# Optimization experiments

Measured on AMD Instinct MI355X. Metric: run time of the kernel, lower is better.

The kernel has to match this reference:

```python
import jax, jax.numpy as jnp
import numpy as np

WIN_H = WIN_W = 7
NUM_HEADS = 6
DIM = 192
HEAD_DIM = DIM // NUM_HEADS
NUM_WIN = 1024
B_ = 8192
N = WIN_H * WIN_W


def _relative_position_index(win_h, win_w):
    coords = np.stack(np.meshgrid(np.arange(win_h), np.arange(win_w), indexing='ij'))  # (2,h,w)
    flat = coords.reshape(2, -1)
    rel = flat[:, :, None] - flat[:, None, :]          # (2, N, N)
    rel = rel.transpose(1, 2, 0).astype(np.int32)      # (N, N, 2)
    rel[:, :, 0] += win_h - 1
    rel[:, :, 1] += win_w - 1
    rel[:, :, 0] *= 2 * win_w - 1
    return rel.sum(-1)                                 # (N, N) in [0, (2h-1)(2w-1))


def setup_inputs() -> dict:
    key = jax.random.key(0)
    ks = jax.random.split(key, 7)
    return {
        'x': jax.random.normal(ks[0], (B_, N, DIM), jnp.float32),
        'mask': jax.random.normal(ks[1], (NUM_WIN, N, N), jnp.float32),
        'qkv_w': jax.random.normal(ks[2], (3 * DIM, DIM), jnp.float32) * 0.02,
        'qkv_b': jax.random.normal(ks[3], (3 * DIM,), jnp.float32) * 0.02,
        'proj_w': jax.random.normal(ks[4], (DIM, DIM), jnp.float32) * 0.02,
        'proj_b': jax.random.normal(ks[5], (DIM,), jnp.float32) * 0.02,
        'rpb_table': jax.random.normal(ks[6], ((2 * WIN_H - 1) * (2 * WIN_W - 1), NUM_HEADS), jnp.float32) * 0.02,
        'rel_index': jnp.asarray(_relative_position_index(WIN_H, WIN_W)),
    }


def reference(x, mask, qkv_w, qkv_b, proj_w, proj_b, rpb_table, rel_index):
    B, n, C = x.shape
    H, hd = NUM_HEADS, HEAD_DIM
    scale = hd ** (-0.5)

    qkv = (x @ qkv_w.T + qkv_b).reshape(B, n, 3, H, hd)
    qkv = jnp.transpose(qkv, (2, 0, 3, 1, 4))          # (3, B, H, N, hd)
    q, k, v = qkv[0], qkv[1], qkv[2]

    attn = jnp.einsum('bhnd,bhmd->bhnm', q * scale, k)  # (B, H, N, N)

    # gathered relative position bias: (N*N,) -> (N, N, H) -> (H, N, N)
    bias = rpb_table[rel_index.reshape(-1)].reshape(n, n, H)
    attn = attn + jnp.transpose(bias, (2, 0, 1))[None]

    num_win = mask.shape[0]
    attn = attn.reshape(B // num_win, num_win, H, n, n) + mask[None, :, None]
    attn = jax.nn.softmax(attn, axis=-1).reshape(B, H, n, n)

    out = jnp.einsum('bhnm,bhmd->bhnd', attn, v)         # (B, H, N, hd)
    out = jnp.transpose(out, (0, 2, 1, 3)).reshape(B, n, H * hd)
    return out @ proj_w.T + proj_b
```

## Files before the change

kernel.cpp:

```cpp
#include <hip/hip_runtime.h>

#define NTOK  49
#define NWIN  1024
#define SCALE 0.17677669529663687f

#define SMEM_BYTES 102400

typedef __bf16 bfx8 __attribute__((ext_vector_type(8)));
typedef float  f32x4 __attribute__((ext_vector_type(4)));
typedef unsigned long long ull;
typedef unsigned int uint;

union BF8 { bfx8 v; ull q[2]; };
union BFU { __bf16 h[4]; ull q; };

__device__ __forceinline__ ull pack4(f32x4 a) {
    BFU u;
    u.h[0] = (__bf16)a[0]; u.h[1] = (__bf16)a[1];
    u.h[2] = (__bf16)a[2]; u.h[3] = (__bf16)a[3];
    return u.q;
}
__device__ __forceinline__ unsigned short f2bf(float f) {
    uint u = __builtin_bit_cast(uint, f);
    u += 0x7fffu + ((u >> 16) & 1u);
    return (unsigned short)(u >> 16);
}
__device__ __forceinline__ f32x4 mfma16(bfx8 a, bfx8 b, f32x4 c) {
    return __builtin_amdgcn_mfma_f32_16x16x32_bf16(a, b, c, 0, 0, 0);
}

extern "C" __global__ void wattn_prep(const float* __restrict__ qkv_w,
                                      const float* __restrict__ proj_w,
                                      const float* __restrict__ rpb,
                                      const int*   __restrict__ rel,
                                      const float* __restrict__ qkv_b,
                                      unsigned short* __restrict__ W1f,
                                      unsigned short* __restrict__ W2p,
                                      float* __restrict__ qkvbs,
                                      float* __restrict__ biasN)
{
    const int i = blockIdx.x * 256 + threadIdx.x;
    if (i < 110592) {
        const int e = i & 7, l = (i >> 3) & 63, f = i >> 9;
        const int kk = f % 6, oct = f / 6;
        const int R = oct * 16 + (l & 15), C = kk * 32 + (l >> 4) * 8 + e;
        float v = qkv_w[R * 192 + C];
        if (oct < 12) v *= SCALE;
        W1f[i] = f2bf(v);
    }
    if (i < 36864) {
        const int e = i & 7, l = (i >> 3) & 63, f = i >> 9;
        const int c2t = f / 6, H = f % 6;
        const int R = c2t * 16 + (l & 15);
        const int C = H * 32 + (e >> 2) * 16 + (l >> 4) * 4 + (e & 3);
        W2p[i] = f2bf(proj_w[R * 192 + C]);
    }
    if (i < 576) qkvbs[i] = (i < 192) ? qkv_b[i] * SCALE : qkv_b[i];
    if (i < 6 * NTOK * 64) {
        const int h = i / (NTOK * 64), ii = (i / 64) % NTOK, j = i % 64;
        biasN[i] = (j < NTOK) ? rpb[rel[ii * NTOK + j] * 6 + h] : -1e30f;
    }
}

extern "C" __global__ void __launch_bounds__(512, 2)
wattn_fused(const float* __restrict__ x,
            const float* __restrict__ mask,
            const float* __restrict__ proj_b,
            const unsigned short* __restrict__ W1f,
            const unsigned short* __restrict__ W2p,
            const float* __restrict__ qkvbs,
            const float* __restrict__ biasN,
            float* __restrict__ out)
{
    __shared__ char smem[SMEM_BYTES];
    char* const XB  = smem;
    char* const OBX = smem;
    char* const QBp = smem + 25600;
    char* const KBp = smem + 50176;
    char* const VTp = smem + 74752;

    const int tid  = threadIdx.x;
    const int wave = tid >> 6;
    const int lane = tid & 63;
    const int g    = lane >> 4;
    const int jn   = lane & 15;
    const int qt   = wave & 3;
    const int hh   = wave >> 2;
    const size_t b = blockIdx.x;

#pragma unroll
    for (int u = 0; u < 3; ++u) {
        const int i = tid + u * 512;
        if (i < 1500)
            *(uint*)(XB + (49 + i / 100) * 400 + (i % 100) * 4) = 0u;
    }
    {
        const float4* xw = (const float4*)(x + b * 9408);
#pragma unroll
        for (int u = 0; u < 5; ++u) {
            const int i = tid + u * 512;
            if (i < 2352) {
                float4 v = xw[i];
                f32x4 vv = {v.x, v.y, v.z, v.w};
                *(ull*)(XB + (i / 48) * 400 + (i % 48) * 8) = pack4(vv);
            }
        }
    }
    __syncthreads();

#pragma unroll
    for (int jj = 0; jj < 2; ++jj) {
        const int pr = wave + 8 * jj;
        const int octA = pr * 2;
        bfx8 wfA[6], wfB[6];
#pragma unroll
        for (int kk = 0; kk < 6; ++kk) {
            wfA[kk] = *(const bfx8*)(W1f + ((size_t)(octA * 6 + kk) * 64 + lane) * 8);
            wfB[kk] = *(const bfx8*)(W1f + ((size_t)((octA + 1) * 6 + kk) * 64 + lane) * 8);
        }
        if (pr < 12) {
            const f32x4 biA = *(const f32x4*)(qkvbs + octA * 16 + 4 * g);
            const f32x4 biB = *(const f32x4*)(qkvbs + (octA + 1) * 16 + 4 * g);
            char* const dst = (pr < 6) ? QBp : KBp;
            const int pp = (pr < 6) ? pr : pr - 6;
#pragma unroll
            for (int tt = 0; tt < 4; ++tt) {
                f32x4 aA = biA, aB = biB;
#pragma unroll
                for (int kk = 0; kk < 6; ++kk) {
                    bfx8 xf = *(const bfx8*)(XB + (tt * 16 + jn) * 400 + kk * 64 + g * 16);
                    aA = mfma16(wfA[kk], xf, aA);
                    aB = mfma16(wfB[kk], xf, aB);
                }
                BF8 o; o.q[0] = pack4(aA); o.q[1] = pack4(aB);
                *(bfx8*)(dst + ((tt * 6 + pp) * 64 + lane) * 16) = o.v;
            }
        } else {
            const float bvA = qkvbs[octA * 16 + jn];
            const float bvB = qkvbs[(octA + 1) * 16 + jn];
            const int cA = octA - 24;
#pragma unroll
            for (int tt = 0; tt < 4; ++tt) {
                f32x4 aA = {bvA, bvA, bvA, bvA};
                f32x4 aB = {bvB, bvB, bvB, bvB};
#pragma unroll
                for (int kk = 0; kk < 6; ++kk) {
                    bfx8 xf = *(const bfx8*)(XB + (tt * 16 + jn) * 400 + kk * 64 + g * 16);
                    aA = mfma16(xf, wfA[kk], aA);
                    aB = mfma16(xf, wfB[kk], aB);
                }
                const int voff = (tt >> 1) * 64 + g * 16 + (tt & 1) * 8;
                *(ull*)(VTp + (cA * 16 + jn) * 144 + voff)       = pack4(aA);
                *(ull*)(VTp + ((cA + 1) * 16 + jn) * 144 + voff) = pack4(aB);
            }
        }
    }
    {
        const int octA = 32 + (wave >> 2) * 2;
        const int tt = wave & 3;
        bfx8 wfA[6], wfB[6];
#pragma unroll
        for (int kk = 0; kk < 6; ++kk) {
            wfA[kk] = *(const bfx8*)(W1f + ((size_t)(octA * 6 + kk) * 64 + lane) * 8);
            wfB[kk] = *(const bfx8*)(W1f + ((size_t)((octA + 1) * 6 + kk) * 64 + lane) * 8);
        }
        const float bvA = qkvbs[octA * 16 + jn];
        const float bvB = qkvbs[(octA + 1) * 16 + jn];
        f32x4 aA = {bvA, bvA, bvA, bvA};
        f32x4 aB = {bvB, bvB, bvB, bvB};
#pragma unroll
        for (int kk = 0; kk < 6; ++kk) {
            bfx8 xf = *(const bfx8*)(XB + (tt * 16 + jn) * 400 + kk * 64 + g * 16);
            aA = mfma16(xf, wfA[kk], aA);
            aB = mfma16(xf, wfB[kk], aB);
        }
        const int cA = octA - 24;
        const int voff = (tt >> 1) * 64 + g * 16 + (tt & 1) * 8;
        *(ull*)(VTp + (cA * 16 + jn) * 144 + voff)       = pack4(aA);
        *(ull*)(VTp + ((cA + 1) * 16 + jn) * 144 + voff) = pack4(aB);
    }
    __syncthreads();

    const int iq = qt * 16 + jn;
    const int ic = iq < NTOK ? iq : NTOK - 1;
    const float* mw = mask + (b & (NWIN - 1)) * (NTOK * NTOK);
    f32x4 mv4[4];
#pragma unroll
    for (int kt = 0; kt < 3; ++kt) {
        float4 t;
        __builtin_memcpy(&t, mw + ic * NTOK + kt * 16 + 4 * g, 16);
        mv4[kt] = (f32x4){t.x, t.y, t.z, t.w};
    }
    {
        const float m48 = mw[ic * NTOK + 48];
        mv4[3] = (f32x4){m48, m48, m48, m48};
    }

    bfx8 qfr = *(const bfx8*)(QBp + ((qt * 6 + hh * 3) * 64 + lane) * 16);
    bfx8 kfc[4];
    f32x4 cic[4];
#pragma unroll
    for (int kt = 0; kt < 4; ++kt) {
        kfc[kt] = *(const bfx8*)(KBp + ((kt * 6 + hh * 3) * 64 + lane) * 16);
        const f32x4 bm4 = *(const f32x4*)(biasN + ((size_t)(hh * 3) * NTOK + ic) * 64 + kt * 16 + 4 * g);
        cic[kt] = bm4 + mv4[kt];
    }

#pragma unroll
    for (int hl = 0; hl < 3; ++hl) {
        const int H = hh * 3 + hl;
        f32x4 p[4];
#pragma unroll
        for (int kt = 0; kt < 4; ++kt)
            p[kt] = mfma16(kfc[kt], qfr, cic[kt]);
        bfx8 qfn, kfn[4];
        f32x4 cin[4];
        if (hl < 2) {
            qfn = *(const bfx8*)(QBp + ((qt * 6 + H + 1) * 64 + lane) * 16);
#pragma unroll
            for (int kt = 0; kt < 4; ++kt) {
                kfn[kt] = *(const bfx8*)(KBp + ((kt * 6 + H + 1) * 64 + lane) * 16);
                const f32x4 bm4 = *(const f32x4*)(biasN + ((size_t)(H + 1) * NTOK + ic) * 64 + kt * 16 + 4 * g);
                cin[kt] = bm4 + mv4[kt];
            }
        }
        float mx = -1e30f;
#pragma unroll
        for (int kt = 0; kt < 4; ++kt)
#pragma unroll
            for (int r = 0; r < 4; ++r) mx = fmaxf(mx, p[kt][r]);
        mx = fmaxf(mx, __shfl_xor(mx, 16));
        mx = fmaxf(mx, __shfl_xor(mx, 32));
        float sum = 0.f;
#pragma unroll
        for (int kt = 0; kt < 4; ++kt)
#pragma unroll
            for (int r = 0; r < 4; ++r) {
                p[kt][r] = __expf(p[kt][r] - mx);
                sum += p[kt][r];
            }
        sum += __shfl_xor(sum, 16);
        sum += __shfl_xor(sum, 32);
        const float inv = 1.f / sum;
        BF8 p01, p23;
        p01.q[0] = pack4(p[0]); p01.q[1] = pack4(p[1]);
        p23.q[0] = pack4(p[2]); p23.q[1] = pack4(p[3]);
#pragma unroll
        for (int ct = 0; ct < 2; ++ct) {
            const int row = H * 32 + ct * 16 + jn;
            bfx8 v0 = *(const bfx8*)(VTp + row * 144 + g * 16);
            bfx8 v1 = *(const bfx8*)(VTp + row * 144 + 64 + g * 16);
            f32x4 o = {0.f, 0.f, 0.f, 0.f};
            o = mfma16(v0, p01.v, o);
            o = mfma16(v1, p23.v, o);
            *(ull*)(OBX + ((qt * 6 + H) * 64 + lane) * 16 + ct * 8) = pack4(o * inv);
        }
        if (hl < 2) {
            qfr = qfn;
#pragma unroll
            for (int kt = 0; kt < 4; ++kt) { kfc[kt] = kfn[kt]; cic[kt] = cin[kt]; }
        }
    }
    __syncthreads();

    const int qh = wave & 1;
    bfx8 obc[2][6];
#pragma unroll
    for (int t2 = 0; t2 < 2; ++t2)
#pragma unroll
        for (int H = 0; H < 6; ++H)
            obc[t2][H] = *(const bfx8*)(OBX + (((qh * 2 + t2) * 6 + H) * 64 + lane) * 16);

    float* outp = out + b * 9408;
#pragma unroll
    for (int t = 0; t < 3; ++t) {
        const int c2t = (wave >> 1) + 4 * t;
        bfx8 wf2[6];
#pragma unroll
        for (int H = 0; H < 6; ++H)
            wf2[H] = *(const bfx8*)(W2p + ((size_t)(c2t * 6 + H) * 64 + lane) * 8);
        const f32x4 pb = *(const f32x4*)(proj_b + c2t * 16 + 4 * g);
#pragma unroll
        for (int t2 = 0; t2 < 2; ++t2) {
            const int qt2 = qh * 2 + t2;
            f32x4 acc = pb;
#pragma unroll
            for (int H = 0; H < 6; ++H)
                acc = mfma16(wf2[H], obc[t2][H], acc);
            const int tok = qt2 * 16 + jn;
            if (tok < NTOK)
                *(f32x4*)(outp + tok * 192 + c2t * 16 + 4 * g) = acc;
        }
    }
}

extern "C" void kernel_launch(void* const* d_in, const int* in_sizes, int n_in,
                              void* d_out, int out_size, void* d_ws, size_t ws_size,
                              hipStream_t stream) {
    const float* x      = (const float*)d_in[0];
    const float* mask   = (const float*)d_in[1];
    const float* qkv_w  = (const float*)d_in[2];
    const float* qkv_b  = (const float*)d_in[3];
    const float* proj_w = (const float*)d_in[4];
    const float* proj_b = (const float*)d_in[5];
    const float* rpb    = (const float*)d_in[6];
    const int*   rel    = (const int*)d_in[7];
    float* outp = (float*)d_out;

    char* ws = (char*)d_ws;
    unsigned short* W1f = (unsigned short*)ws;
    unsigned short* W2p = (unsigned short*)(ws + 221184);
    float* qkvbs        = (float*)(ws + 221184 + 73728);
    float* biasN        = (float*)(ws + 221184 + 73728 + 2304);

    wattn_prep<<<432, 256, 0, stream>>>(qkv_w, proj_w, rpb, rel, qkv_b,
                                        W1f, W2p, qkvbs, biasN);
    wattn_fused<<<8192, 512, 0, stream>>>(x, mask, proj_b,
                                          W1f, W2p, qkvbs, biasN, outp);
}
```

Baseline: 420.0 us.

## Process two windows per block and prefetch next window's input into registers

Each block now handles two consecutive windows instead of one, halving the grid. While the first window runs its output projection, the second window's x tile is loaded from global memory into registers, so the load latency overlaps compute. MFMA sections are also wrapped in s_setprio raises to favour matrix issue across waves. The cost is more register pressure from the prefetch buffer and fewer blocks to spread across CUs.

```diff
diff --git a/kernel.cpp b/kernel.cpp
--- a/kernel.cpp
+++ b/kernel.cpp
@@ -86,211 +86,238 @@
     const int jn   = lane & 15;
     const int qt   = wave & 3;
     const int hh   = wave >> 2;
-    const size_t b = blockIdx.x;
-
-#pragma unroll
-    for (int u = 0; u < 3; ++u) {
-        const int i = tid + u * 512;
-        if (i < 1500)
-            *(uint*)(XB + (49 + i / 100) * 400 + (i % 100) * 4) = 0u;
-    }
-    {
-        const float4* xw = (const float4*)(x + b * 9408);
-#pragma unroll
-        for (int u = 0; u < 5; ++u) {
+    const size_t b2 = (size_t)blockIdx.x * 2;
+
+    float4 xr[5];
+
+    for (int w = 0; w < 2; ++w) {
+#pragma unroll
+        for (int u = 0; u < 3; ++u) {
             const int i = tid + u * 512;
-            if (i < 2352) {
-                float4 v = xw[i];
-                f32x4 vv = {v.x, v.y, v.z, v.w};
-                *(ull*)(XB + (i / 48) * 400 + (i % 48) * 8) = pack4(vv);
-            }
-        }
-    }
-    __syncthreads();
-
-#pragma unroll
-    for (int jj = 0; jj < 2; ++jj) {
-        const int pr = wave + 8 * jj;
-        const int octA = pr * 2;
-        bfx8 wfA[6], wfB[6];
-#pragma unroll
-        for (int kk = 0; kk < 6; ++kk) {
-            wfA[kk] = *(const bfx8*)(W1f + ((size_t)(octA * 6 + kk) * 64 + lane) * 8);
-            wfB[kk] = *(const bfx8*)(W1f + ((size_t)((octA + 1) * 6 + kk) * 64 + lane) * 8);
-        }
-        if (pr < 12) {
-            const f32x4 biA = *(const f32x4*)(qkvbs + octA * 16 + 4 * g);
-            const f32x4 biB = *(const f32x4*)(qkvbs + (octA + 1) * 16 + 4 * g);
-            char* const dst = (pr < 6) ? QBp : KBp;
-            const int pp = (pr < 6) ? pr : pr - 6;
-#pragma unroll
-            for (int tt = 0; tt < 4; ++tt) {
-                f32x4 aA = biA, aB = biB;
-#pragma unroll
-                for (int kk = 0; kk < 6; ++kk) {
-                    bfx8 xf = *(const bfx8*)(XB + (tt * 16 + jn) * 400 + kk * 64 + g * 16);
-                    aA = mfma16(wfA[kk], xf, aA);
-                    aB = mfma16(wfB[kk], xf, aB);
-                }
-                BF8 o; o.q[0] = pack4(aA); o.q[1] = pack4(aB);
-                *(bfx8*)(dst + ((tt * 6 + pp) * 64 + lane) * 16) = o.v;
+            if (i < 1500)
+                *(uint*)(XB + (49 + i / 100) * 400 + (i % 100) * 4) = 0u;
+        }
+        if (w == 0) {
+            const float4* xw = (const float4*)(x + b2 * 9408);
+#pragma unroll
+            for (int u = 0; u < 5; ++u) {
+                const int i = tid + u * 512;
+                if (i < 2352) {
+                    float4 v = xw[i];
+                    f32x4 vv = {v.x, v.y, v.z, v.w};
+                    *(ull*)(XB + (i / 48) * 400 + (i % 48) * 8) = pack4(vv);
+                }
             }
         } else {
+#pragma unroll
+            for (int u = 0; u < 5; ++u) {
+                const int i = tid + u * 512;
+                if (i < 2352) {
+                    f32x4 vv = {xr[u].x, xr[u].y, xr[u].z, xr[u].w};
+                    *(ull*)(XB + (i / 48) * 400 + (i % 48) * 8) = pack4(vv);
+                }
+            }
+        }
+        __syncthreads();
+
+#pragma unroll
+        for (int jj = 0; jj < 2; ++jj) {
+            const int pr = wave + 8 * jj;
+            const int octA = pr * 2;
+            bfx8 wfA[6], wfB[6];
+#pragma unroll
+            for (int kk = 0; kk < 6; ++kk) {
+                wfA[kk] = *(const bfx8*)(W1f + ((size_t)(octA * 6 + kk) * 64 + lane) * 8);
+                wfB[kk] = *(const bfx8*)(W1f + ((size_t)((octA + 1) * 6 + kk) * 64 + lane) * 8);
+            }
+            if (pr < 12) {
+                const f32x4 biA = *(const f32x4*)(qkvbs + octA * 16 + 4 * g);
+                const f32x4 biB = *(const f32x4*)(qkvbs + (octA + 1) * 16 + 4 * g);
+                char* const dst = (pr < 6) ? QBp : KBp;
+                const int pp = (pr < 6) ? pr : pr - 6;
+#pragma unroll
+                for (int tt = 0; tt < 4; ++tt) {
+                    f32x4 aA = biA, aB = biB;
+#pragma unroll
+                    for (int kk = 0; kk < 6; ++kk) {
+                        bfx8 xf = *(const bfx8*)(XB + (tt * 16 + jn) * 400 + kk * 64 + g * 16);
+                        aA = mfma16(wfA[kk], xf, aA);
+                        aB = mfma16(wfB[kk], xf, aB);
+                    }
+                    BF8 o; o.q[0] = pack4(aA); o.q[1] = pack4(aB);
+                    *(bfx8*)(dst + ((tt * 6 + pp) * 64 + lane) * 16) = o.v;
+                }
+            } else {
+                const float bvA = qkvbs[octA * 16 + jn];
+                const float bvB = qkvbs[(octA + 1) * 16 + jn];
+                const int cA = octA - 24;
+#pragma unroll
+                for (int tt = 0; tt < 4; ++tt) {
+                    f32x4 aA = {bvA, bvA, bvA, bvA};
+                    f32x4 aB = {bvB, bvB, bvB, bvB};
+#pragma unroll
+                    for (int kk = 0; kk < 6; ++kk) {
+                        bfx8 xf = *(const bfx8*)(XB + (tt * 16 + jn) * 400 + kk * 64 + g * 16);
+                        aA = mfma16(xf, wfA[kk], aA);
+                        aB = mfma16(xf, wfB[kk], aB);
+                    }
+                    const int voff = (tt >> 1) * 64 + g * 16 + (tt & 1) * 8;
+                    *(ull*)(VTp + (cA * 16 + jn) * 144 + voff)       = pack4(aA);
+                    *(ull*)(VTp + ((cA + 1) * 16 + jn) * 144 + voff) = pack4(aB);
+                }
+            }
+        }
+        {
+            const int octA = 32 + (wave >> 2) * 2;
+            const int tt = wave & 3;
+            bfx8 wfA[6], wfB[6];
+#pragma unroll
+            for (int kk = 0; kk < 6; ++kk) {
+                wfA[kk] = *(const bfx8*)(W1f + ((size_t)(octA * 6 + kk) * 64 + lane) * 8);
+                wfB[kk] = *(const bfx8*)(W1f + ((size_t)((octA + 1) * 6 + kk) * 64 + lane) * 8);
+            }
             const float bvA = qkvbs[octA * 16 + jn];
             const float bvB = qkvbs[(octA + 1) * 16 + jn];
+            f32x4 aA = {bvA, bvA, bvA, bvA};
+            f32x4 aB = {bvB, bvB, bvB, bvB};
+#pragma unroll
+            for (int kk = 0; kk < 6; ++kk) {
+                bfx8 xf = *(const bfx8*)(XB + (tt * 16 + jn) * 400 + kk * 64 + g * 16);
+                aA = mfma16(xf, wfA[kk], aA);
+                aB = mfma16(xf, wfB[kk], aB);
+            }
             const int cA = octA - 24;
-#pragma unroll
-            for (int tt = 0; tt < 4; ++tt) {
-                f32x4 aA = {bvA, bvA, bvA, bvA};
-                f32x4 aB = {bvB, bvB, bvB, bvB};
-#pragma unroll
-                for (int kk = 0; kk < 6; ++kk) {
-                    bfx8 xf = *(const bfx8*)(XB + (tt * 16 + jn) * 400 + kk * 64 + g * 16);
-                    aA = mfma16(xf, wfA[kk], aA);
-                    aB = mfma16(xf, wfB[kk], aB);
-                }
-                const int voff = (tt >> 1) * 64 + g * 16 + (tt & 1) * 8;
-                *(ull*)(VTp + (cA * 16 + jn) * 144 + voff)       = pack4(aA);
-                *(ull*)(VTp + ((cA + 1) * 16 + jn) * 144 + voff) = pack4(aB);
-            }
-        }
-    }
-    {
-        const int octA = 32 + (wave >> 2) * 2;
-        const int tt = wave & 3;
-        bfx8 wfA[6], wfB[6];
-#pragma unroll
-        for (int kk = 0; kk < 6; ++kk) {
-            wfA[kk] = *(const bfx8*)(W1f + ((size_t)(octA * 6 + kk) * 64 + lane) * 8);
-            wfB[kk] = *(const bfx8*)(W1f + ((size_t)((octA + 1) * 6 + kk) * 64 + lane) * 8);
-        }
-        const float bvA = qkvbs[octA * 16 + jn];
-        const float bvB = qkvbs[(octA + 1) * 16 + jn];
-        f32x4 aA = {bvA, bvA, bvA, bvA};
-        f32x4 aB = {bvB, bvB, bvB, bvB};
-#pragma unroll
-        for (int kk = 0; kk < 6; ++kk) {
-            bfx8 xf = *(const bfx8*)(XB + (tt * 16 + jn) * 400 + kk * 64 + g * 16);
-            aA = mfma16(xf, wfA[kk], aA);
-            aB = mfma16(xf, wfB[kk], aB);
-        }
-        const int cA = octA - 24;
-        const int voff = (tt >> 1) * 64 + g * 16 + (tt & 1) * 8;
-        *(ull*)(VTp + (cA * 16 + jn) * 144 + voff)       = pack4(aA);
-        *(ull*)(VTp + ((cA + 1) * 16 + jn) * 144 + voff) = pack4(aB);
-    }
-    __syncthreads();
-
-    const int iq = qt * 16 + jn;
-    const int ic = iq < NTOK ? iq : NTOK - 1;
-    const float* mw = mask + (b & (NWIN - 1)) * (NTOK * NTOK);
-    f32x4 mv4[4];
-#pragma unroll
-    for (int kt = 0; kt < 3; ++kt) {
-        float4 t;
-        __builtin_memcpy(&t, mw + ic * NTOK + kt * 16 + 4 * g, 16);
-        mv4[kt] = (f32x4){t.x, t.y, t.z, t.w};
-    }
-    {
-        const float m48 = mw[ic * NTOK + 48];
-        mv4[3] = (f32x4){m48, m48, m48, m48};
-    }
-
-    bfx8 qfr = *(const bfx8*)(QBp + ((qt * 6 + hh * 3) * 64 + lane) * 16);
-    bfx8 kfc[4];
-    f32x4 cic[4];
-#pragma unroll
-    for (int kt = 0; kt < 4; ++kt) {
-        kfc[kt] = *(const bfx8*)(KBp + ((kt * 6 + hh * 3) * 64 + lane) * 16);
-        const f32x4 bm4 = *(const f32x4*)(biasN + ((size_t)(hh * 3) * NTOK + ic) * 64 + kt * 16 + 4 * g);
-        cic[kt] = bm4 + mv4[kt];
-    }
-
-#pragma unroll
-    for (int hl = 0; hl < 3; ++hl) {
-        const int H = hh * 3 + hl;
-        f32x4 p[4];
-#pragma unroll
-        for (int kt = 0; kt < 4; ++kt)
-            p[kt] = mfma16(kfc[kt], qfr, cic[kt]);
-        bfx8 qfn, kfn[4];
-        f32x4 cin[4];
-        if (hl < 2) {
-            qfn = *(const bfx8*)(QBp + ((qt * 6 + H + 1) * 64 + lane) * 16);
-#pragma unroll
-            for (int kt = 0; kt < 4; ++kt) {
-                kfn[kt] = *(const bfx8*)(KBp + ((kt * 6 + H + 1) * 64 + lane) * 16);
-                const f32x4 bm4 = *(const f32x4*)(biasN + ((size_t)(H + 1) * NTOK + ic) * 64 + kt * 16 + 4 * g);
-                cin[kt] = bm4 + mv4[kt];
-            }
-        }
-        float mx = -1e30f;
-#pragma unroll
-        for (int kt = 0; kt < 4; ++kt)
-#pragma unroll
-            for (int r = 0; r < 4; ++r) mx = fmaxf(mx, p[kt][r]);
-        mx = fmaxf(mx, __shfl_xor(mx, 16));
-        mx = fmaxf(mx, __shfl_xor(mx, 32));
-        float sum = 0.f;
-#pragma unroll
-        for (int kt = 0; kt < 4; ++kt)
-#pragma unroll
-            for (int r = 0; r < 4; ++r) {
-                p[kt][r] = __expf(p[kt][r] - mx);
-                sum += p[kt][r];
-            }
-        sum += __shfl_xor(sum, 16);
-        sum += __shfl_xor(sum, 32);
-        const float inv = 1.f / sum;
-        BF8 p01, p23;
-        p01.q[0] = pack4(p[0]); p01.q[1] = pack4(p[1]);
-        p23.q[0] = pack4(p[2]); p23.q[1] = pack4(p[3]);
-#pragma unroll
-        for (int ct = 0; ct < 2; ++ct) {
-            const int row = H * 32 + ct * 16 + jn;
-            bfx8 v0 = *(const bfx8*)(VTp + row * 144 + g * 16);
-            bfx8 v1 = *(const bfx8*)(VTp + row * 144 + 64 + g * 16);
-            f32x4 o = {0.f, 0.f, 0.f, 0.f};
-            o = mfma16(v0, p01.v, o);
-            o = mfma16(v1, p23.v, o);
-            *(ull*)(OBX + ((qt * 6 + H) * 64 + lane) * 16 + ct * 8) = pack4(o * inv);
-        }
-        if (hl < 2) {
-            qfr = qfn;
-#pragma unroll
-            for (int kt = 0; kt < 4; ++kt) { kfc[kt] = kfn[kt]; cic[kt] = cin[kt]; }
-        }
-    }
-    __syncthreads();
-
-    const int qh = wave & 1;
-    bfx8 obc[2][6];
-#pragma unroll
-    for (int t2 = 0; t2 < 2; ++t2)
-#pragma unroll
-        for (int H = 0; H < 6; ++H)
-            obc[t2][H] = *(const bfx8*)(OBX + (((qh * 2 + t2) * 6 + H) * 64 + lane) * 16);
-
-    float* outp = out + b * 9408;
-#pragma unroll
-    for (int t = 0; t < 3; ++t) {
-        const int c2t = (wave >> 1) + 4 * t;
-        bfx8 wf2[6];
-#pragma unroll
-        for (int H = 0; H < 6; ++H)
-            wf2[H] = *(const bfx8*)(W2p + ((size_t)(c2t * 6 + H) * 64 + lane) * 8);
-        const f32x4 pb = *(const f32x4*)(proj_b + c2t * 16 + 4 * g);
-#pragma unroll
-        for (int t2 = 0; t2 < 2; ++t2) {
-            const int qt2 = qh * 2 + t2;
-            f32x4 acc = pb;
+            const int voff = (tt >> 1) * 64 + g * 16 + (tt & 1) * 8;
+            *(ull*)(VTp + (cA * 16 + jn) * 144 + voff)       = pack4(aA);
+            *(ull*)(VTp + ((cA + 1) * 16 + jn) * 144 + voff) = pack4(aB);
+        }
+        __syncthreads();
+
+        const int iq = qt * 16 + jn;
+        const int ic = iq < NTOK ? iq : NTOK - 1;
+        const float* mw = mask + ((b2 + w) & (NWIN - 1)) * (NTOK * NTOK);
+        f32x4 mv4[4];
+#pragma unroll
+        for (int kt = 0; kt < 3; ++kt) {
+            float4 t;
+            __builtin_memcpy(&t, mw + ic * NTOK + kt * 16 + 4 * g, 16);
+            mv4[kt] = (f32x4){t.x, t.y, t.z, t.w};
+        }
+        {
+            const float m48 = mw[ic * NTOK + 48];
+            mv4[3] = (f32x4){m48, m48, m48, m48};
+        }
+
+        bfx8 qfr = *(const bfx8*)(QBp + ((qt * 6 + hh * 3) * 64 + lane) * 16);
+        bfx8 kfc[4];
+        f32x4 cic[4];
+#pragma unroll
+        for (int kt = 0; kt < 4; ++kt) {
+            kfc[kt] = *(const bfx8*)(KBp + ((kt * 6 + hh * 3) * 64 + lane) * 16);
+            const f32x4 bm4 = *(const f32x4*)(biasN + ((size_t)(hh * 3) * NTOK + ic) * 64 + kt * 16 + 4 * g);
+            cic[kt] = bm4 + mv4[kt];
+        }
+
+#pragma unroll
+        for (int hl = 0; hl < 3; ++hl) {
+            const int H = hh * 3 + hl;
+            f32x4 p[4];
+            __builtin_amdgcn_s_setprio(1);
+#pragma unroll
+            for (int kt = 0; kt < 4; ++kt)
+                p[kt] = mfma16(kfc[kt], qfr, cic[kt]);
+            __builtin_amdgcn_s_setprio(0);
+            bfx8 qfn, kfn[4];
+            f32x4 cin[4];
+            if (hl < 2) {
+                qfn = *(const bfx8*)(QBp + ((qt * 6 + H + 1) * 64 + lane) * 16);
+#pragma unroll
+                for (int kt = 0; kt < 4; ++kt) {
+                    kfn[kt] = *(const bfx8*)(KBp + ((kt * 6 + H + 1) * 64 + lane) * 16);
+                    const f32x4 bm4 = *(const f32x4*)(biasN + ((size_t)(H + 1) * NTOK + ic) * 64 + kt * 16 + 4 * g);
+                    cin[kt] = bm4 + mv4[kt];
+                }
+            }
+            float mx = -1e30f;
+#pragma unroll
+            for (int kt = 0; kt < 4; ++kt)
+#pragma unroll
+                for (int r = 0; r < 4; ++r) mx = fmaxf(mx, p[kt][r]);
+            mx = fmaxf(mx, __shfl_xor(mx, 16));
+            mx = fmaxf(mx, __shfl_xor(mx, 32));
+            float sum = 0.f;
+#pragma unroll
+            for (int kt = 0; kt < 4; ++kt)
+#pragma unroll
+                for (int r = 0; r < 4; ++r) {
+                    p[kt][r] = __expf(p[kt][r] - mx);
+                    sum += p[kt][r];
+                }
+            sum += __shfl_xor(sum, 16);
+            sum += __shfl_xor(sum, 32);
+            const float inv = 1.f / sum;
+            BF8 p01, p23;
+            p01.q[0] = pack4(p[0]); p01.q[1] = pack4(p[1]);
+            p23.q[0] = pack4(p[2]); p23.q[1] = pack4(p[3]);
+            __builtin_amdgcn_s_setprio(1);
+#pragma unroll
+            for (int ct = 0; ct < 2; ++ct) {
+                const int row = H * 32 + ct * 16 + jn;
+                bfx8 v0 = *(const bfx8*)(VTp + row * 144 + g * 16);
+                bfx8 v1 = *(const bfx8*)(VTp + row * 144 + 64 + g * 16);
+                f32x4 o = {0.f, 0.f, 0.f, 0.f};
+                o = mfma16(v0, p01.v, o);
+                o = mfma16(v1, p23.v, o);
+                *(ull*)(OBX + ((qt * 6 + H) * 64 + lane) * 16 + ct * 8) = pack4(o * inv);
+            }
+            __builtin_amdgcn_s_setprio(0);
+            if (hl < 2) {
+                qfr = qfn;
+#pragma unroll
+                for (int kt = 0; kt < 4; ++kt) { kfc[kt] = kfn[kt]; cic[kt] = cin[kt]; }
+            }
+        }
+        __syncthreads();
+
+        if (w == 0) {
+            const float4* xw1 = (const float4*)(x + (b2 + 1) * 9408);
+#pragma unroll
+            for (int u = 0; u < 5; ++u) {
+                const int i = tid + u * 512;
+                xr[u] = (i < 2352) ? xw1[i] : (float4){0.f, 0.f, 0.f, 0.f};
+            }
+        }
+
+        const int qh = wave & 1;
+        bfx8 obc[2][6];
+#pragma unroll
+        for (int t2 = 0; t2 < 2; ++t2)
 #pragma unroll
             for (int H = 0; H < 6; ++H)
-                acc = mfma16(wf2[H], obc[t2][H], acc);
-            const int tok = qt2 * 16 + jn;
-            if (tok < NTOK)
-                *(f32x4*)(outp + tok * 192 + c2t * 16 + 4 * g) = acc;
-        }
+                obc[t2][H] = *(const bfx8*)(OBX + (((qh * 2 + t2) * 6 + H) * 64 + lane) * 16);
+
+        float* outp = out + (b2 + w) * 9408;
+#pragma unroll
+        for (int t = 0; t < 3; ++t) {
+            const int c2t = (wave >> 1) + 4 * t;
+            bfx8 wf2[6];
+#pragma unroll
+            for (int H = 0; H < 6; ++H)
+                wf2[H] = *(const bfx8*)(W2p + ((size_t)(c2t * 6 + H) * 64 + lane) * 8);
+            const f32x4 pb = *(const f32x4*)(proj_b + c2t * 16 + 4 * g);
+#pragma unroll
+            for (int t2 = 0; t2 < 2; ++t2) {
+                const int qt2 = qh * 2 + t2;
+                f32x4 acc = pb;
+#pragma unroll
+                for (int H = 0; H < 6; ++H)
+                    acc = mfma16(wf2[H], obc[t2][H], acc);
+                const int tok = qt2 * 16 + jn;
+                if (tok < NTOK)
+                    *(f32x4*)(outp + tok * 192 + c2t * 16 + 4 * g) = acc;
+            }
+        }
+        if (w == 0) __syncthreads();
     }
 }
 
@@ -315,6 +342,6 @@
 
     wattn_prep<<<432, 256, 0, stream>>>(qkv_w, proj_w, rpb, rel, qkv_b,
                                         W1f, W2p, qkvbs, biasN);
-    wattn_fused<<<8192, 512, 0, stream>>>(x, mask, proj_b,
+    wattn_fused<<<4096, 512, 0, stream>>>(x, mask, proj_b,
                                           W1f, W2p, qkvbs, biasN, outp);
 }
```

Result: slower. 1.121 ms (+167.0%).
